# Optimization experiments

Measured on AMD Instinct MI355X. Metric: run time of the kernel, lower is better.

## Reference

```python
import jax, jax.numpy as jnp
import numpy as np

B, S, D = 8, 2048, 128
H = 4
HD = D // H  # 32


def setup_inputs() -> dict:
    key = jax.random.key(0)
    k1, k2, k3 = jax.random.split(key, 3)
    x = jax.random.normal(k1, (B, S, D), dtype=jnp.float32)
    w_attn = jax.random.normal(k2, (D, 3 * D), dtype=jnp.float32) * (1.0 / np.sqrt(D))
    w_proj = jax.random.normal(k3, (D, D), dtype=jnp.float32) * (1.0 / np.sqrt(D))
    return {"x": x, "w_attn": w_attn, "w_proj": w_proj}


def reference(x, w_attn, w_proj):
    b, s, d = x.shape
    qkv = x @ w_attn  # [B,S,3D]
    q, k, v = jnp.split(qkv, 3, axis=-1)
    # [B,H,S,HD]
    q = q.reshape(b, s, H, HD).transpose(0, 2, 1, 3)
    k = k.reshape(b, s, H, HD).transpose(0, 2, 1, 3)
    v = v.reshape(b, s, H, HD).transpose(0, 2, 1, 3)
    scale = 1.0 / jnp.sqrt(jnp.asarray(HD, dtype=x.dtype))
    scores = jnp.einsum('bhqd,bhkd->bhqk', q, k) * scale  # [B,H,S,S]
    causal = jnp.tril(jnp.ones((s, s), dtype=bool))
    scores = jnp.where(causal, scores, jnp.finfo(x.dtype).min)
    attn = jax.nn.softmax(scores, axis=-1)
    out = jnp.einsum('bhqk,bhkd->bhqd', attn, v)  # [B,H,S,HD]
    out = out.transpose(0, 2, 1, 3).reshape(b, s, d)
    out = out @ w_proj  # c_proj; dropout is identity in eval
    return out
```

## Files before the change

### kernel.cpp

```cpp
#include <hip/hip_runtime.h>
#include <hip/hip_bf16.h>

#define B_  8
#define S_  2048
#define D_  128
#define H_  4
#define HD_ 32
#define BH_ (B_ * H_)

typedef __bf16 bf16x8 __attribute__((ext_vector_type(8)));
typedef float f32x16 __attribute__((ext_vector_type(16)));

__device__ inline bf16x8 ld8(const __hip_bfloat16* p) {
    return *reinterpret_cast<const bf16x8*>(p);
}
__device__ inline unsigned cvtpk(float lo, float hi) {
    unsigned r;
    asm("v_cvt_pk_bf16_f32 %0, %1, %2" : "=v"(r) : "v"(lo), "v"(hi));
    return r;
}
__device__ inline void swap32(unsigned &a, unsigned &b) {
    asm("v_permlane32_swap_b32 %0, %1" : "+v"(a), "+v"(b));
}
__device__ inline float ex2(float x) { return __builtin_amdgcn_exp2f(x); }

__global__ __launch_bounds__(256) void conv_w(const float* __restrict__ wa,
                                              const float* __restrict__ wp,
                                              __hip_bfloat16* __restrict__ wt,
                                              __hip_bfloat16* __restrict__ wpt) {
    __shared__ float tile[32][33];
    int bid = blockIdx.x;
    const float* src;
    __hip_bfloat16* dst;
    int N, k0, n0;
    if (bid < 48) { src = wa; dst = wt;  N = 384; k0 = (bid / 12) * 32; n0 = (bid % 12) * 32; }
    else { bid -= 48; src = wp; dst = wpt; N = 128; k0 = (bid / 4) * 32; n0 = (bid % 4) * 32; }
    const int r = threadIdx.x >> 5, c = threadIdx.x & 31;
#pragma unroll
    for (int j = 0; j < 4; ++j)
        tile[r + 8 * j][c] = src[(k0 + r + 8 * j) * N + n0 + c];
    __syncthreads();
#pragma unroll
    for (int j = 0; j < 4; ++j)
        dst[(n0 + r + 8 * j) * 128 + k0 + c] = __float2bfloat16(tile[c][r + 8 * j]);
}

__global__ __launch_bounds__(256) void qkv_mfma(const float* __restrict__ x,
                                                const __hip_bfloat16* __restrict__ wt,
                                                __hip_bfloat16* __restrict__ Qb,
                                                __hip_bfloat16* __restrict__ Kb,
                                                __hip_bfloat16* __restrict__ Vt) {
    const int mt   = blockIdx.x;
    const int wave = threadIdx.x >> 6;
    const int lane = threadIdx.x & 63;
    const int lq   = lane & 31;
    const int hi   = lane >> 5;
    const int m0   = mt * 32;

    const float* ax = x + (m0 + lq) * 128 + 8 * hi;
    const __hip_bfloat16* bq = wt + ((      wave * 32) + lq) * 128 + 8 * hi;
    const __hip_bfloat16* bk = wt + ((128 + wave * 32) + lq) * 128 + 8 * hi;
    const __hip_bfloat16* bv = wt + ((256 + wave * 32) + lq) * 128 + 8 * hi;

    f32x16 aq = {}, ak = {}, av = {};

    float4 x0a = *reinterpret_cast<const float4*>(ax);
    float4 x1a = *reinterpret_cast<const float4*>(ax + 4);
    bf16x8 bqa = ld8(bq), bka = ld8(bk), bva = ld8(bv);
    float4 x0b = *reinterpret_cast<const float4*>(ax + 16);
    float4 x1b = *reinterpret_cast<const float4*>(ax + 20);
    bf16x8 bqb = ld8(bq + 16), bkb = ld8(bk + 16), bvb = ld8(bv + 16);

#pragma unroll
    for (int ks = 0; ks < 8; ++ks) {
        const float4 cx0 = x0a, cx1 = x1a;
        const bf16x8 cbq = bqa, cbk = bka, cbv = bva;
        x0a = x0b; x1a = x1b; bqa = bqb; bka = bkb; bva = bvb;
        if (ks < 6) {
            x0b = *reinterpret_cast<const float4*>(ax + 16 * (ks + 2));
            x1b = *reinterpret_cast<const float4*>(ax + 16 * (ks + 2) + 4);
            bqb = ld8(bq + 16 * (ks + 2));
            bkb = ld8(bk + 16 * (ks + 2));
            bvb = ld8(bv + 16 * (ks + 2));
        }
        union { unsigned u[4]; bf16x8 v; } af;
        af.u[0] = cvtpk(cx0.x, cx0.y); af.u[1] = cvtpk(cx0.z, cx0.w);
        af.u[2] = cvtpk(cx1.x, cx1.y); af.u[3] = cvtpk(cx1.z, cx1.w);
        aq = __builtin_amdgcn_mfma_f32_32x32x16_bf16(cbq, af.v, aq, 0, 0, 0);
        ak = __builtin_amdgcn_mfma_f32_32x32x16_bf16(cbk, af.v, ak, 0, 0, 0);
        av = __builtin_amdgcn_mfma_f32_32x32x16_bf16(af.v, cbv, av, 0, 0, 0);
    }

    const int b  = m0 >> 11;
    const int s0 = m0 & (S_ - 1);
    const int bh = b * H_ + wave;
    const float qs = 0.2550052557342824f;

    __hip_bfloat16* qrow = Qb + (bh * S_ + s0 + lq) * HD_ + 4 * hi;
    __hip_bfloat16* krow = Kb + (bh * S_ + s0 + lq) * HD_ + 4 * hi;
#pragma unroll
    for (int g = 0; g < 4; ++g) {
        union { __hip_bfloat16 h[4]; ushort4 u; } pq, pk;
#pragma unroll
        for (int j = 0; j < 4; ++j) {
            pq.h[j] = __float2bfloat16(aq[4 * g + j] * qs);
            pk.h[j] = __float2bfloat16(ak[4 * g + j]);
        }
        *reinterpret_cast<ushort4*>(qrow + 8 * g) = pq.u;
        *reinterpret_cast<ushort4*>(krow + 8 * g) = pk.u;
    }
    __hip_bfloat16* vbase = Vt + (bh * HD_ + lq) * S_ + s0;
#pragma unroll
    for (int g = 0; g < 4; ++g) {
        union { __hip_bfloat16 h[4]; ushort4 u; } pv;
#pragma unroll
        for (int j = 0; j < 4; ++j) pv.h[j] = __float2bfloat16(av[4 * g + j]);
        *reinterpret_cast<ushort4*>(vbase + 8 * g + 4 * hi) = pv.u;
    }
}

__global__ __launch_bounds__(256, 4) void fattn_kernel(
    const __hip_bfloat16* __restrict__ Qb,
    const __hip_bfloat16* __restrict__ Kb,
    const __hip_bfloat16* __restrict__ Vt,
    __hip_bfloat16* __restrict__ AOb)
{
    __shared__ float Ol[4][64][33];
    __shared__ float Ll[4][64];

    const int bh   = blockIdx.x & 31;
    const int qt2  = 31 - (blockIdx.x >> 5);
    const int tid  = threadIdx.x;
    const int wv   = tid >> 6;
    const int lane = tid & 63;
    const int lq   = lane & 31;
    const int hi   = lane >> 5;

    const int q0  = qt2 * 64;
    const int qtA = 2 * qt2;
    const int qtB = qtA + 1;
    const int nt  = qtB + 1;

    const __hip_bfloat16* qrowA = Qb + (bh * S_ + q0 + lq) * HD_ + 8 * hi;
    const __hip_bfloat16* qrowB = qrowA + 32 * HD_;
    const bf16x8 qfA0 = ld8(qrowA), qfA1 = ld8(qrowA + 16);
    const bf16x8 qfB0 = ld8(qrowB), qfB1 = ld8(qrowB + 16);

    const __hip_bfloat16* kp = Kb + bh * S_ * HD_ + lq * HD_ + 8 * hi;
    const __hip_bfloat16* vp = Vt + (bh * HD_ + lq) * S_ + 8 * hi;

    f32x16 oaccA = {}, oaccB = {};
    float lsumA = 0.f, lsumB = 0.f;

    bf16x8 k0a = {}, k1a = {}, v0a = {}, v1a = {};
    if (wv < nt) {
        k0a = ld8(kp + wv * 32 * HD_); k1a = ld8(kp + wv * 32 * HD_ + 16);
        v0a = ld8(vp + wv * 32);       v1a = ld8(vp + wv * 32 + 16);
    }

    for (int t = wv; t < nt; t += 4) {
        const bf16x8 ck0 = k0a, ck1 = k1a, cv0 = v0a, cv1 = v1a;
        if (t + 4 < nt) {
            const __hip_bfloat16* kn = kp + (t + 4) * 32 * HD_;
            const __hip_bfloat16* vn = vp + (t + 4) * 32;
            k0a = ld8(kn); k1a = ld8(kn + 16);
            v0a = ld8(vn); v1a = ld8(vn + 16);
        }

        if (t <= qtA) {
            __builtin_amdgcn_s_setprio(1);
            f32x16 s = {};
            s = __builtin_amdgcn_mfma_f32_32x32x16_bf16(ck0, qfA0, s, 0, 0, 0);
            s = __builtin_amdgcn_mfma_f32_32x32x16_bf16(ck1, qfA1, s, 0, 0, 0);
            __builtin_amdgcn_s_setprio(0);

            if (t == qtA) {
#pragma unroll
                for (int r = 0; r < 16; ++r) {
                    const int kloc = (r & 3) + 8 * (r >> 2) + 4 * hi;
                    s[r] = (kloc > lq) ? -1e30f : s[r];
                }
            }
#pragma unroll
            for (int r = 0; r < 16; ++r) s[r] = ex2(s[r]);
            {
                float p0 = (s[0] + s[1]) + (s[2] + s[3]);
                float p1 = (s[4] + s[5]) + (s[6] + s[7]);
                float p2 = (s[8] + s[9]) + (s[10] + s[11]);
                float p3 = (s[12] + s[13]) + (s[14] + s[15]);
                lsumA += (p0 + p1) + (p2 + p3);
            }
            unsigned a0 = cvtpk(s[0], s[1]),   a1 = cvtpk(s[2], s[3]);
            unsigned a2 = cvtpk(s[4], s[5]),   a3 = cvtpk(s[6], s[7]);
            swap32(a0, a2); swap32(a1, a3);
            unsigned b0 = cvtpk(s[8], s[9]),   b1 = cvtpk(s[10], s[11]);
            unsigned b2 = cvtpk(s[12], s[13]), b3 = cvtpk(s[14], s[15]);
            swap32(b0, b2); swap32(b1, b3);
            union { unsigned u[4]; bf16x8 v; } pb0, pb1;
            pb0.u[0] = a0; pb0.u[1] = a1; pb0.u[2] = a2; pb0.u[3] = a3;
            pb1.u[0] = b0; pb1.u[1] = b1; pb1.u[2] = b2; pb1.u[3] = b3;

            __builtin_amdgcn_s_setprio(1);
            oaccA = __builtin_amdgcn_mfma_f32_32x32x16_bf16(cv0, pb0.v, oaccA, 0, 0, 0);
            oaccA = __builtin_amdgcn_mfma_f32_32x32x16_bf16(cv1, pb1.v, oaccA, 0, 0, 0);
            __builtin_amdgcn_s_setprio(0);
        }

        {
            __builtin_amdgcn_s_setprio(1);
            f32x16 s = {};
            s = __builtin_amdgcn_mfma_f32_32x32x16_bf16(ck0, qfB0, s, 0, 0, 0);
            s = __builtin_amdgcn_mfma_f32_32x32x16_bf16(ck1, qfB1, s, 0, 0, 0);
            __builtin_amdgcn_s_setprio(0);

            if (t == qtB) {
#pragma unroll
                for (int r = 0; r < 16; ++r) {
                    const int kloc = (r & 3) + 8 * (r >> 2) + 4 * hi;
                    s[r] = (kloc > lq) ? -1e30f : s[r];
                }
            }
#pragma unroll
            for (int r = 0; r < 16; ++r) s[r] = ex2(s[r]);
            {
                float p0 = (s[0] + s[1]) + (s[2] + s[3]);
                float p1 = (s[4] + s[5]) + (s[6] + s[7]);
                float p2 = (s[8] + s[9]) + (s[10] + s[11]);
                float p3 = (s[12] + s[13]) + (s[14] + s[15]);
                lsumB += (p0 + p1) + (p2 + p3);
            }
            unsigned a0 = cvtpk(s[0], s[1]),   a1 = cvtpk(s[2], s[3]);
            unsigned a2 = cvtpk(s[4], s[5]),   a3 = cvtpk(s[6], s[7]);
            swap32(a0, a2); swap32(a1, a3);
            unsigned b0 = cvtpk(s[8], s[9]),   b1 = cvtpk(s[10], s[11]);
            unsigned b2 = cvtpk(s[12], s[13]), b3 = cvtpk(s[14], s[15]);
            swap32(b0, b2); swap32(b1, b3);
            union { unsigned u[4]; bf16x8 v; } pb0, pb1;
            pb0.u[0] = a0; pb0.u[1] = a1; pb0.u[2] = a2; pb0.u[3] = a3;
            pb1.u[0] = b0; pb1.u[1] = b1; pb1.u[2] = b2; pb1.u[3] = b3;

            __builtin_amdgcn_s_setprio(1);
            oaccB = __builtin_amdgcn_mfma_f32_32x32x16_bf16(cv0, pb0.v, oaccB, 0, 0, 0);
            oaccB = __builtin_amdgcn_mfma_f32_32x32x16_bf16(cv1, pb1.v, oaccB, 0, 0, 0);
            __builtin_amdgcn_s_setprio(0);
        }
    }

    lsumA += __shfl_xor(lsumA, 32);
    lsumB += __shfl_xor(lsumB, 32);

#pragma unroll
    for (int r = 0; r < 16; ++r) {
        const int d = (r & 3) + 8 * (r >> 2) + 4 * hi;
        Ol[wv][lq][d]      = oaccA[r];
        Ol[wv][32 + lq][d] = oaccB[r];
    }
    if (hi == 0) { Ll[wv][lq] = lsumA; Ll[wv][32 + lq] = lsumB; }
    __syncthreads();

    const int q  = tid >> 2;
    const int d0 = (tid & 3) * 8;
    const float lst = Ll[0][q] + Ll[1][q] + Ll[2][q] + Ll[3][q];
    const float inv = 1.f / lst;

    const int b = bh >> 2, h = bh & 3;
    __hip_bfloat16* orow = AOb + (b * S_ + q0 + q) * D_ + h * HD_ + d0;
#pragma unroll
    for (int g = 0; g < 2; ++g) {
        union { __hip_bfloat16 h4[4]; ushort4 u; } st;
#pragma unroll
        for (int j = 0; j < 4; ++j) {
            const int d = d0 + 4 * g + j;
            const float o = Ol[0][q][d] + Ol[1][q][d] + Ol[2][q][d] + Ol[3][q][d];
            st.h4[j] = __float2bfloat16(o * inv);
        }
        *reinterpret_cast<ushort4*>(orow + 4 * g) = st.u;
    }
}

__global__ __launch_bounds__(256) void proj_mfma(const __hip_bfloat16* __restrict__ AOb,
                                                 const __hip_bfloat16* __restrict__ wpt,
                                                 float* __restrict__ out) {
    const int m0   = blockIdx.x * 32;
    const int wave = threadIdx.x >> 6;
    const int lane = threadIdx.x & 63;
    const int lq   = lane & 31;
    const int hi   = lane >> 5;
    const int n0   = wave * 32;

    const __hip_bfloat16* ap = AOb + (m0 + lq) * 128 + 8 * hi;
    const __hip_bfloat16* bp = wpt + (n0 + lq) * 128 + 8 * hi;

    bf16x8 A[8], Bf[8];
#pragma unroll
    for (int ks = 0; ks < 8; ++ks) {
        A[ks]  = ld8(ap + 16 * ks);
        Bf[ks] = ld8(bp + 16 * ks);
    }

    f32x16 acc = {};
#pragma unroll
    for (int ks = 0; ks < 8; ++ks)
        acc = __builtin_amdgcn_mfma_f32_32x32x16_bf16(Bf[ks], A[ks], acc, 0, 0, 0);

    float* orow = out + (m0 + lq) * 128 + n0 + 4 * hi;
#pragma unroll
    for (int g = 0; g < 4; ++g) {
        float4 st = make_float4(acc[4 * g], acc[4 * g + 1], acc[4 * g + 2], acc[4 * g + 3]);
        *reinterpret_cast<float4*>(orow + 8 * g) = st;
    }
}

extern "C" void kernel_launch(void* const* d_in, const int* in_sizes, int n_in,
                              void* d_out, int out_size, void* d_ws, size_t ws_size,
                              hipStream_t stream) {
    const float* x      = (const float*)d_in[0];
    const float* w_attn = (const float*)d_in[1];
    const float* w_proj = (const float*)d_in[2];
    float* out = (float*)d_out;

    char* ws = (char*)d_ws;
    __hip_bfloat16* Qb  = (__hip_bfloat16*)(ws);
    __hip_bfloat16* Kb  = (__hip_bfloat16*)(ws + (4  << 20));
    __hip_bfloat16* Vt  = (__hip_bfloat16*)(ws + (8  << 20));
    __hip_bfloat16* AOb = (__hip_bfloat16*)(ws + (12 << 20));
    __hip_bfloat16* wt  = (__hip_bfloat16*)(ws + (16 << 20));
    __hip_bfloat16* wpt = (__hip_bfloat16*)(ws + (16 << 20) + (128 << 10));

    conv_w<<<64, 256, 0, stream>>>(w_attn, w_proj, wt, wpt);
    qkv_mfma<<<512, 256, 0, stream>>>(x, wt, Qb, Kb, Vt);
    fattn_kernel<<<BH_ * 32, 256, 0, stream>>>(Qb, Kb, Vt, AOb);
    proj_mfma<<<512, 256, 0, stream>>>(AOb, wpt, out);
}
```

Baseline: 51.02 us.

## Fuse weight bf16 conversion into QKV and projection GEMM kernels via LDS

Removes the separate conv_w launch by having each QKV and projection block convert and transpose its needed weight slice from fp32 into shared memory. QKV blocks are regrouped so each block handles one head across four 32-row tiles, letting all waves share one LDS weight slice. This saves a kernel launch and a workspace round trip. In exchange every block redoes the weight conversion with strided global reads and a barrier, and the explicit register prefetch pipelining is dropped.

```diff
diff --git a/kernel.cpp b/kernel.cpp
--- a/kernel.cpp
+++ b/kernel.cpp
@@ -24,76 +24,55 @@
 }
 __device__ inline float ex2(float x) { return __builtin_amdgcn_exp2f(x); }
 
-__global__ __launch_bounds__(256) void conv_w(const float* __restrict__ wa,
-                                              const float* __restrict__ wp,
-                                              __hip_bfloat16* __restrict__ wt,
-                                              __hip_bfloat16* __restrict__ wpt) {
-    __shared__ float tile[32][33];
-    int bid = blockIdx.x;
-    const float* src;
-    __hip_bfloat16* dst;
-    int N, k0, n0;
-    if (bid < 48) { src = wa; dst = wt;  N = 384; k0 = (bid / 12) * 32; n0 = (bid % 12) * 32; }
-    else { bid -= 48; src = wp; dst = wpt; N = 128; k0 = (bid / 4) * 32; n0 = (bid % 4) * 32; }
-    const int r = threadIdx.x >> 5, c = threadIdx.x & 31;
-#pragma unroll
-    for (int j = 0; j < 4; ++j)
-        tile[r + 8 * j][c] = src[(k0 + r + 8 * j) * N + n0 + c];
-    __syncthreads();
-#pragma unroll
-    for (int j = 0; j < 4; ++j)
-        dst[(n0 + r + 8 * j) * 128 + k0 + c] = __float2bfloat16(tile[c][r + 8 * j]);
-}
-
 __global__ __launch_bounds__(256) void qkv_mfma(const float* __restrict__ x,
-                                                const __hip_bfloat16* __restrict__ wt,
+                                                const float* __restrict__ wa,
                                                 __hip_bfloat16* __restrict__ Qb,
                                                 __hip_bfloat16* __restrict__ Kb,
                                                 __hip_bfloat16* __restrict__ Vt) {
-    const int mt   = blockIdx.x;
-    const int wave = threadIdx.x >> 6;
-    const int lane = threadIdx.x & 63;
+    __shared__ __align__(16) __hip_bfloat16 wl[96][136];
+
+    const int head = blockIdx.x & 3;
+    const int mblk = blockIdx.x >> 2;
+    const int tid  = threadIdx.x;
+
+    for (int idx = tid; idx < 128 * 96; idx += 256) {
+        const int k = idx / 96;
+        const int c = idx - k * 96;
+        const int sec = c >> 5, nloc = c & 31;
+        wl[c][k] = __float2bfloat16(wa[k * 384 + sec * 128 + head * 32 + nloc]);
+    }
+    __syncthreads();
+
+    const int wave = tid >> 6;
+    const int lane = tid & 63;
     const int lq   = lane & 31;
     const int hi   = lane >> 5;
-    const int m0   = mt * 32;
+    const int m0   = mblk * 128 + wave * 32;
 
     const float* ax = x + (m0 + lq) * 128 + 8 * hi;
-    const __hip_bfloat16* bq = wt + ((      wave * 32) + lq) * 128 + 8 * hi;
-    const __hip_bfloat16* bk = wt + ((128 + wave * 32) + lq) * 128 + 8 * hi;
-    const __hip_bfloat16* bv = wt + ((256 + wave * 32) + lq) * 128 + 8 * hi;
+    const __hip_bfloat16* bq = &wl[lq][8 * hi];
+    const __hip_bfloat16* bk = &wl[32 + lq][8 * hi];
+    const __hip_bfloat16* bv = &wl[64 + lq][8 * hi];
 
     f32x16 aq = {}, ak = {}, av = {};
-
-    float4 x0a = *reinterpret_cast<const float4*>(ax);
-    float4 x1a = *reinterpret_cast<const float4*>(ax + 4);
-    bf16x8 bqa = ld8(bq), bka = ld8(bk), bva = ld8(bv);
-    float4 x0b = *reinterpret_cast<const float4*>(ax + 16);
-    float4 x1b = *reinterpret_cast<const float4*>(ax + 20);
-    bf16x8 bqb = ld8(bq + 16), bkb = ld8(bk + 16), bvb = ld8(bv + 16);
-
 #pragma unroll
     for (int ks = 0; ks < 8; ++ks) {
-        const float4 cx0 = x0a, cx1 = x1a;
-        const bf16x8 cbq = bqa, cbk = bka, cbv = bva;
-        x0a = x0b; x1a = x1b; bqa = bqb; bka = bkb; bva = bvb;
-        if (ks < 6) {
-            x0b = *reinterpret_cast<const float4*>(ax + 16 * (ks + 2));
-            x1b = *reinterpret_cast<const float4*>(ax + 16 * (ks + 2) + 4);
-            bqb = ld8(bq + 16 * (ks + 2));
-            bkb = ld8(bk + 16 * (ks + 2));
-            bvb = ld8(bv + 16 * (ks + 2));
-        }
+        float4 x0 = *reinterpret_cast<const float4*>(ax + 16 * ks);
+        float4 x1 = *reinterpret_cast<const float4*>(ax + 16 * ks + 4);
         union { unsigned u[4]; bf16x8 v; } af;
-        af.u[0] = cvtpk(cx0.x, cx0.y); af.u[1] = cvtpk(cx0.z, cx0.w);
-        af.u[2] = cvtpk(cx1.x, cx1.y); af.u[3] = cvtpk(cx1.z, cx1.w);
-        aq = __builtin_amdgcn_mfma_f32_32x32x16_bf16(cbq, af.v, aq, 0, 0, 0);
-        ak = __builtin_amdgcn_mfma_f32_32x32x16_bf16(cbk, af.v, ak, 0, 0, 0);
-        av = __builtin_amdgcn_mfma_f32_32x32x16_bf16(af.v, cbv, av, 0, 0, 0);
+        af.u[0] = cvtpk(x0.x, x0.y); af.u[1] = cvtpk(x0.z, x0.w);
+        af.u[2] = cvtpk(x1.x, x1.y); af.u[3] = cvtpk(x1.z, x1.w);
+        const bf16x8 wqf = ld8(bq + 16 * ks);
+        const bf16x8 wkf = ld8(bk + 16 * ks);
+        const bf16x8 wvf = ld8(bv + 16 * ks);
+        aq = __builtin_amdgcn_mfma_f32_32x32x16_bf16(wqf, af.v, aq, 0, 0, 0);
+        ak = __builtin_amdgcn_mfma_f32_32x32x16_bf16(wkf, af.v, ak, 0, 0, 0);
+        av = __builtin_amdgcn_mfma_f32_32x32x16_bf16(af.v, wvf, av, 0, 0, 0);
     }
 
     const int b  = m0 >> 11;
     const int s0 = m0 & (S_ - 1);
-    const int bh = b * H_ + wave;
+    const int bh = b * H_ + head;
     const float qs = 0.2550052557342824f;
 
     __hip_bfloat16* qrow = Qb + (bh * S_ + s0 + lq) * HD_ + 4 * hi;
@@ -279,29 +258,34 @@
 }
 
 __global__ __launch_bounds__(256) void proj_mfma(const __hip_bfloat16* __restrict__ AOb,
-                                                 const __hip_bfloat16* __restrict__ wpt,
+                                                 const float* __restrict__ wp,
                                                  float* __restrict__ out) {
+    __shared__ __align__(16) __hip_bfloat16 wl[128][136];
+
+    const int tid = threadIdx.x;
+    for (int idx = tid; idx < 128 * 128; idx += 256) {
+        const int k = idx >> 7, n = idx & 127;
+        wl[n][k] = __float2bfloat16(wp[idx]);
+    }
+    __syncthreads();
+
     const int m0   = blockIdx.x * 32;
-    const int wave = threadIdx.x >> 6;
-    const int lane = threadIdx.x & 63;
+    const int wave = tid >> 6;
+    const int lane = tid & 63;
     const int lq   = lane & 31;
     const int hi   = lane >> 5;
     const int n0   = wave * 32;
 
     const __hip_bfloat16* ap = AOb + (m0 + lq) * 128 + 8 * hi;
-    const __hip_bfloat16* bp = wpt + (n0 + lq) * 128 + 8 * hi;
-
-    bf16x8 A[8], Bf[8];
+    const __hip_bfloat16* bp = &wl[n0 + lq][8 * hi];
+
+    f32x16 acc = {};
 #pragma unroll
     for (int ks = 0; ks < 8; ++ks) {
-        A[ks]  = ld8(ap + 16 * ks);
-        Bf[ks] = ld8(bp + 16 * ks);
-    }
-
-    f32x16 acc = {};
-#pragma unroll
-    for (int ks = 0; ks < 8; ++ks)
-        acc = __builtin_amdgcn_mfma_f32_32x32x16_bf16(Bf[ks], A[ks], acc, 0, 0, 0);
+        const bf16x8 af = ld8(ap + 16 * ks);
+        const bf16x8 bf = ld8(bp + 16 * ks);
+        acc = __builtin_amdgcn_mfma_f32_32x32x16_bf16(bf, af, acc, 0, 0, 0);
+    }
 
     float* orow = out + (m0 + lq) * 128 + n0 + 4 * hi;
 #pragma unroll
@@ -324,11 +308,8 @@
     __hip_bfloat16* Kb  = (__hip_bfloat16*)(ws + (4  << 20));
     __hip_bfloat16* Vt  = (__hip_bfloat16*)(ws + (8  << 20));
     __hip_bfloat16* AOb = (__hip_bfloat16*)(ws + (12 << 20));
-    __hip_bfloat16* wt  = (__hip_bfloat16*)(ws + (16 << 20));
-    __hip_bfloat16* wpt = (__hip_bfloat16*)(ws + (16 << 20) + (128 << 10));
-
-    conv_w<<<64, 256, 0, stream>>>(w_attn, w_proj, wt, wpt);
-    qkv_mfma<<<512, 256, 0, stream>>>(x, wt, Qb, Kb, Vt);
+
+    qkv_mfma<<<512, 256, 0, stream>>>(x, w_attn, Qb, Kb, Vt);
     fattn_kernel<<<BH_ * 32, 256, 0, stream>>>(Qb, Kb, Vt, AOb);
-    proj_mfma<<<512, 256, 0, stream>>>(AOb, wpt, out);
-}
+    proj_mfma<<<512, 256, 0, stream>>>(AOb, w_proj, out);
+}
```

Result: faster. 47.08 us (-7.7%).
